# Kernel tuning notes

Hardware: AMD Instinct MI355X
Metric: run time of the kernel (lower is better)

The kernel has to match this reference:

```python
import jax, jax.numpy as jnp
import numpy as np

B, T, IN, OUT = 8, 2048, 1024, 512
DT, TAU = 1.0, 20.0


def setup_inputs() -> dict:
    key = jax.random.key(0)
    k1, k2 = jax.random.split(key)
    x = jax.random.normal(k1, (B, T, IN), jnp.float32)
    lim = 1.0 / np.sqrt(IN)
    weight = jax.random.uniform(k2, (OUT, IN), jnp.float32, -lim, lim)
    bias = jnp.zeros((OUT,), jnp.float32)
    # fixed tau trainer: decay = exp(-dt / tau) per output feature
    decay = jnp.full((OUT,), float(np.exp(-DT / TAU)), jnp.float32)
    return {"input_tensor": x, "weight": weight, "bias": bias, "decay": decay}


def reference(input_tensor, weight, bias, decay):
    # Hoist the time-invariant GEMM out of the recurrence: [B,T,OUT]
    current = jnp.einsum('bti,oi->bto', input_tensor, weight) + bias
    v0 = jnp.zeros((input_tensor.shape[0], weight.shape[0]), input_tensor.dtype)

    def step(v_tm1, c_t):
        v_t = decay * v_tm1 + (1.0 - decay) * c_t
        return v_t, v_t

    # scan over time axis: [T,B,OUT]
    _, outs = jax.lax.scan(step, v0, jnp.swapaxes(current, 0, 1))
    outputs = jnp.swapaxes(outs, 0, 1)  # [B,T,OUT]
    states = jnp.concatenate([v0[:, None, :], outputs], axis=1)[None]  # [1,B,T+1,OUT]
    return outputs, states
```

## Files before the change

kernel.cpp:

```cpp
#include <hip/hip_runtime.h>
#include <hip/hip_bf16.h>
#include <cstddef>
#include <cstdint>

#define BB    8
#define TT    2048
#define KIN   1024
#define NOUT  512
#define CHUNK 32
#define NCHUNK (TT / CHUNK)

#define BM 128
#define BN 64
#define BK 32
#define NKSTEP (KIN / BK)

typedef __attribute__((ext_vector_type(4))) float          f32x4;
typedef __attribute__((ext_vector_type(4))) unsigned int   u32x4;
typedef _Float16 f16x8 __attribute__((ext_vector_type(8)));

__global__ __launch_bounds__(256) void conv_f16_kernel(
    const float* __restrict__ src, _Float16* __restrict__ dst, int n8) {
  int i = blockIdx.x * blockDim.x + threadIdx.x;
  const int stride = gridDim.x * blockDim.x;
  for (; i < n8; i += stride) {
    float4 x0 = reinterpret_cast<const float4*>(src)[2 * i];
    float4 x1 = reinterpret_cast<const float4*>(src)[2 * i + 1];
    f16x8 h;
    h[0] = (_Float16)x0.x; h[1] = (_Float16)x0.y;
    h[2] = (_Float16)x0.z; h[3] = (_Float16)x0.w;
    h[4] = (_Float16)x1.x; h[5] = (_Float16)x1.y;
    h[6] = (_Float16)x1.z; h[7] = (_Float16)x1.w;
    reinterpret_cast<f16x8*>(dst)[i] = h;
  }
}

#define G2L(gp, sp)                                                        \
  __builtin_amdgcn_global_load_lds(                                       \
      (const __attribute__((address_space(1))) void*)(gp),                \
      (__attribute__((address_space(3))) void*)(sp), 16, 0, 0)

__global__ __launch_bounds__(256, 4) void gemm_f16(
    const float* __restrict__ X, const _Float16* __restrict__ Wh,
    const float* __restrict__ bias, const float* __restrict__ decay,
    float* __restrict__ C, float* __restrict__ vend) {
  __shared__ __align__(16) unsigned char smem[8192 + 2 * 4096];

  const int tid  = threadIdx.x;
  const int wave = tid >> 6;
  const int lane = tid & 63;
  const int m0 = blockIdx.x * BM;
  const int n0 = blockIdx.y * BN;
  const int wm = (wave >> 1) * 64;
  const int wn = (wave & 1) * 32;
  const int frow = lane & 15;
  const int g    = lane >> 4;

  const int ar = wave * 8 + (lane >> 3);
  const int as = lane & 7;
  const float* gA = X + (size_t)(m0 + ar) * KIN + as * 4;
  const int awb = ((as >> 1) ^ ((ar >> 1) & 3)) * 16 + (as & 1) * 8;

  const int brow = wave * 16 + (lane >> 2);
  const int sgB  = (lane & 3) ^ ((lane >> 3) & 3);
  const _Float16* gB = Wh + (size_t)(n0 + brow) * KIN + sgB * 8;

  const int swzr = (g ^ ((frow >> 1) & 3)) << 4;

  f32x4 acc[4][2] = {};
  f32x4 ra0, ra1, ra2, ra3;

  ra0 = *reinterpret_cast<const f32x4*>(gA);
  ra1 = *reinterpret_cast<const f32x4*>(gA + (size_t)32 * KIN);
  ra2 = *reinterpret_cast<const f32x4*>(gA + (size_t)64 * KIN);
  ra3 = *reinterpret_cast<const f32x4*>(gA + (size_t)96 * KIN);
  G2L(gB, smem + 8192 + wave * 1024);

  for (int t = 0; t < NKSTEP; ++t) {
    __syncthreads();

    {
      uint2 w;
      w.x = __builtin_bit_cast(unsigned int, __builtin_amdgcn_cvt_pkrtz(ra0[0], ra0[1]));
      w.y = __builtin_bit_cast(unsigned int, __builtin_amdgcn_cvt_pkrtz(ra0[2], ra0[3]));
      *reinterpret_cast<uint2*>(smem + (ar +  0) * 64 + awb) = w;
      w.x = __builtin_bit_cast(unsigned int, __builtin_amdgcn_cvt_pkrtz(ra1[0], ra1[1]));
      w.y = __builtin_bit_cast(unsigned int, __builtin_amdgcn_cvt_pkrtz(ra1[2], ra1[3]));
      *reinterpret_cast<uint2*>(smem + (ar + 32) * 64 + awb) = w;
      w.x = __builtin_bit_cast(unsigned int, __builtin_amdgcn_cvt_pkrtz(ra2[0], ra2[1]));
      w.y = __builtin_bit_cast(unsigned int, __builtin_amdgcn_cvt_pkrtz(ra2[2], ra2[3]));
      *reinterpret_cast<uint2*>(smem + (ar + 64) * 64 + awb) = w;
      w.x = __builtin_bit_cast(unsigned int, __builtin_amdgcn_cvt_pkrtz(ra3[0], ra3[1]));
      w.y = __builtin_bit_cast(unsigned int, __builtin_amdgcn_cvt_pkrtz(ra3[2], ra3[3]));
      *reinterpret_cast<uint2*>(smem + (ar + 96) * 64 + awb) = w;
    }
    __syncthreads();

    if (t + 1 < NKSTEP) {
      const int k0 = (t + 1) * BK;
      ra0 = *reinterpret_cast<const f32x4*>(gA + k0);
      ra1 = *reinterpret_cast<const f32x4*>(gA + (size_t)32 * KIN + k0);
      ra2 = *reinterpret_cast<const f32x4*>(gA + (size_t)64 * KIN + k0);
      ra3 = *reinterpret_cast<const f32x4*>(gA + (size_t)96 * KIN + k0);
      G2L(gB + k0, smem + 8192 + ((t + 1) & 1) * 4096 + wave * 1024);
    }

    const unsigned char* bB = smem + 8192 + (t & 1) * 4096;
    f16x8 af[4];
#pragma unroll
    for (int mi = 0; mi < 4; ++mi)
      af[mi] = *reinterpret_cast<const f16x8*>(smem + (wm + mi * 16 + frow) * 64 + swzr);
#pragma unroll
    for (int ni = 0; ni < 2; ++ni) {
      f16x8 bf = *reinterpret_cast<const f16x8*>(bB + (wn + ni * 16 + frow) * 64 + swzr);
#pragma unroll
      for (int mi = 0; mi < 4; ++mi)
        acc[mi][ni] = __builtin_amdgcn_mfma_f32_16x16x32_f16(af[mi], bf, acc[mi][ni], 0, 0, 0);
    }
  }

  const int colb = n0 + wn + frow;
  const int rowb = m0 + wm + (g << 2);
  const float bv0 = bias[colb];
  const float bv1 = bias[colb + 16];
#pragma unroll
  for (int mi = 0; mi < 4; ++mi) {
#pragma unroll
    for (int r = 0; r < 4; ++r) {
      C[(size_t)(rowb + mi * 16 + r) * NOUT + colb]      = acc[mi][0][r] + bv0;
      C[(size_t)(rowb + mi * 16 + r) * NOUT + colb + 16] = acc[mi][1][r] + bv1;
    }
  }

  {
    const float d0 = decay[colb];
    const float d1 = decay[colb + 16];
    float rr[2][2];
#pragma unroll
    for (int ni = 0; ni < 2; ++ni) {
      const float d = ni ? d1 : d0;
      const float bv = ni ? bv1 : bv0;
      const float omd = 1.0f - d;
      const float dd = d * d, d4 = dd * dd, d8 = d4 * d4;
      const float d16 = d8 * d8, d12 = d8 * d4;
      const float dpg = (g == 0) ? d12 : (g == 1) ? d8 : (g == 2) ? d4 : 1.0f;
      float s[4];
#pragma unroll
      for (int mi = 0; mi < 4; ++mi) {
        float v = acc[mi][ni][0] + bv;
        v = v * d + (acc[mi][ni][1] + bv);
        v = v * d + (acc[mi][ni][2] + bv);
        v = v * d + (acc[mi][ni][3] + bv);
        s[mi] = omd * v;
      }
      float ulo = dpg * (s[0] * d16 + s[1]);
      float uhi = dpg * (s[2] * d16 + s[3]);
      ulo += __shfl_xor(ulo, 16); ulo += __shfl_xor(ulo, 32);
      uhi += __shfl_xor(uhi, 16); uhi += __shfl_xor(uhi, 32);
      rr[0][ni] = ulo; rr[1][ni] = uhi;
    }
    const int b     = m0 >> 11;
    const int clo   = ((m0 & (TT - 1)) >> 5) + (wm >> 5);
    const float val = rr[g >> 1][g & 1];
    const int chunk = clo + (g >> 1);
    const int col   = n0 + wn + frow + (g & 1) * 16;
    vend[((size_t)b * NCHUNK + chunk) * NOUT + col] = val;
  }
}

__global__ __launch_bounds__(256) void gemm_f32_64x64(
    const float* __restrict__ X, const float* __restrict__ W,
    const float* __restrict__ bias, float* __restrict__ C) {
  __shared__ float As[16][65];
  __shared__ float Bs[16][65];
  const int m0  = blockIdx.y * 64;
  const int n0  = blockIdx.x * 64;
  const int tid = threadIdx.x;
  const int tx  = tid & 15;
  const int ty  = tid >> 4;
  const int lr  = tid >> 2;
  const int lk  = (tid & 3) << 2;
  float acc[4][4] = {};
  const float* xa = X + (size_t)(m0 + lr) * KIN + lk;
  const float* wb = W + (size_t)(n0 + lr) * KIN + lk;
  for (int k0 = 0; k0 < KIN; k0 += 16) {
    float4 av = *reinterpret_cast<const float4*>(xa + k0);
    float4 bv = *reinterpret_cast<const float4*>(wb + k0);
    As[lk + 0][lr] = av.x; As[lk + 1][lr] = av.y;
    As[lk + 2][lr] = av.z; As[lk + 3][lr] = av.w;
    Bs[lk + 0][lr] = bv.x; Bs[lk + 1][lr] = bv.y;
    Bs[lk + 2][lr] = bv.z; Bs[lk + 3][lr] = bv.w;
    __syncthreads();
#pragma unroll
    for (int k = 0; k < 16; ++k) {
      float a[4], b[4];
#pragma unroll
      for (int i = 0; i < 4; ++i) a[i] = As[k][ty * 4 + i];
#pragma unroll
      for (int j = 0; j < 4; ++j) b[j] = Bs[k][tx * 4 + j];
#pragma unroll
      for (int i = 0; i < 4; ++i)
#pragma unroll
        for (int j = 0; j < 4; ++j) acc[i][j] += a[i] * b[j];
    }
    __syncthreads();
  }
  const int n = n0 + tx * 4;
  float4 bv = *reinterpret_cast<const float4*>(&bias[n]);
#pragma unroll
  for (int i = 0; i < 4; ++i) {
    const int m = m0 + ty * 4 + i;
    float4 r;
    r.x = acc[i][0] + bv.x; r.y = acc[i][1] + bv.y;
    r.z = acc[i][2] + bv.z; r.w = acc[i][3] + bv.w;
    *reinterpret_cast<float4*>(&C[(size_t)m * NOUT + n]) = r;
  }
}

__global__ __launch_bounds__(512) void scan_chunks(
    const float* __restrict__ vend, const float* __restrict__ decay,
    float* __restrict__ vinit) {
  const int b = blockIdx.x;
  const int o = threadIdx.x;
  const float d = decay[o];
  float d2 = d * d, d4 = d2 * d2, d8 = d4 * d4, d16 = d8 * d8;
  const float dL = d16 * d16;
  float V = 0.0f;
  for (int c = 0; c < NCHUNK; ++c) {
    const size_t idx = ((size_t)b * NCHUNK + c) * NOUT + o;
    vinit[idx] = V;
    V = dL * V + vend[idx];
  }
}

__global__ __launch_bounds__(512) void scan_fixup(
    float* __restrict__ C, float* __restrict__ states,
    const float* __restrict__ decay, const float* __restrict__ vinit) {
  const int b = blockIdx.x / NCHUNK;
  const int c = blockIdx.x % NCHUNK;
  const int o = threadIdx.x;
  const float d   = decay[o];
  const float omd = 1.0f - d;
  float v = vinit[((size_t)b * NCHUNK + c) * NOUT + o];
  size_t obase = ((size_t)b * TT + (size_t)c * CHUNK) * NOUT + o;
  size_t sbase = ((size_t)b * (TT + 1) + (size_t)c * CHUNK + 1) * NOUT + o;
#pragma unroll 4
  for (int k = 0; k < CHUNK; ++k) {
    v = d * v + omd * C[obase + (size_t)k * NOUT];
    C[obase + (size_t)k * NOUT]      = v;
    states[sbase + (size_t)k * NOUT] = v;
  }
  if (c == 0) states[((size_t)b * (TT + 1)) * NOUT + o] = 0.0f;
}

__global__ __launch_bounds__(512) void scan_seq(
    float* __restrict__ C, float* __restrict__ states,
    const float* __restrict__ decay) {
  const int b = blockIdx.x;
  const int o = threadIdx.x;
  const float d   = decay[o];
  const float omd = 1.0f - d;
  float v = 0.0f;
  states[((size_t)b * (TT + 1)) * NOUT + o] = 0.0f;
  for (int t = 0; t < TT; ++t) {
    const size_t oi = ((size_t)b * TT + t) * NOUT + o;
    float x = C[oi];
    v = d * v + omd * x;
    C[oi] = v;
    states[((size_t)b * (TT + 1) + t + 1) * NOUT + o] = v;
  }
}

extern "C" void kernel_launch(void* const* d_in, const int* in_sizes, int n_in,
                              void* d_out, int out_size, void* d_ws, size_t ws_size,
                              hipStream_t stream) {
  const float* x     = (const float*)d_in[0];
  const float* w     = (const float*)d_in[1];
  const float* bias  = (const float*)d_in[2];
  const float* decay = (const float*)d_in[3];

  float* out    = (float*)d_out;
  float* states = out + (size_t)BB * TT * NOUT;

  const size_t szW = (size_t)NOUT * KIN;
  const size_t scan_elems = (size_t)BB * NCHUNK * NOUT;
  const size_t need = szW * sizeof(_Float16)
                    + 2 * scan_elems * sizeof(float);

  if (ws_size >= need) {
    _Float16* Wh = (_Float16*)d_ws;
    float* vend  = (float*)(Wh + szW);
    float* vinit = vend + scan_elems;

    conv_f16_kernel<<<256, 256, 0, stream>>>(w, Wh, (int)(szW / 8));
    gemm_f16<<<dim3((BB * TT) / BM, NOUT / BN), 256, 0, stream>>>(
        x, Wh, bias, decay, out, vend);
    scan_chunks<<<BB, NOUT, 0, stream>>>(vend, decay, vinit);
    scan_fixup <<<BB * NCHUNK, NOUT, 0, stream>>>(out, states, decay, vinit);
  } else {
    gemm_f32_64x64<<<dim3(NOUT / 64, (BB * TT) / 64), 256, 0, stream>>>(x, w, bias, out);
    scan_seq<<<BB, NOUT, 0, stream>>>(out, states, decay);
  }
}
```

Before: 76.68 us.

## Double-buffer A and B tiles in LDS with two-stage register prefetch

```diff
diff --git a/kernel.cpp b/kernel.cpp
--- a/kernel.cpp
+++ b/kernel.cpp
@@ -14,6 +14,9 @@
 #define BN 64
 #define BK 32
 #define NKSTEP (KIN / BK)
+
+#define ABUF 8192
+#define BBUF 4096
 
 typedef __attribute__((ext_vector_type(4))) float          f32x4;
 typedef __attribute__((ext_vector_type(4))) unsigned int   u32x4;
@@ -35,16 +38,11 @@
   }
 }
 
-#define G2L(gp, sp)                                                        \
-  __builtin_amdgcn_global_load_lds(                                       \
-      (const __attribute__((address_space(1))) void*)(gp),                \
-      (__attribute__((address_space(3))) void*)(sp), 16, 0, 0)
-
 __global__ __launch_bounds__(256, 4) void gemm_f16(
     const float* __restrict__ X, const _Float16* __restrict__ Wh,
     const float* __restrict__ bias, const float* __restrict__ decay,
     float* __restrict__ C, float* __restrict__ vend) {
-  __shared__ __align__(16) unsigned char smem[8192 + 2 * 4096];
+  __shared__ __align__(16) unsigned char smem[2 * ABUF + 2 * BBUF];
 
   const int tid  = threadIdx.x;
   const int wave = tid >> 6;
@@ -56,67 +54,92 @@
   const int frow = lane & 15;
   const int g    = lane >> 4;
 
+  unsigned char* bufA0 = smem;
+  unsigned char* bufA1 = smem + ABUF;
+  unsigned char* bufB0 = smem + 2 * ABUF;
+  unsigned char* bufB1 = smem + 2 * ABUF + BBUF;
+
   const int ar = wave * 8 + (lane >> 3);
   const int as = lane & 7;
   const float* gA = X + (size_t)(m0 + ar) * KIN + as * 4;
   const int awb = ((as >> 1) ^ ((ar >> 1) & 3)) * 16 + (as & 1) * 8;
 
-  const int brow = wave * 16 + (lane >> 2);
-  const int sgB  = (lane & 3) ^ ((lane >> 3) & 3);
-  const _Float16* gB = Wh + (size_t)(n0 + brow) * KIN + sgB * 8;
+  const int br = wave * 16 + (lane >> 2);
+  const int sb = lane & 3;
+  const _Float16* gB = Wh + (size_t)(n0 + br) * KIN + (sb ^ ((br >> 1) & 3)) * 8;
+  const int bwb = br * 64 + sb * 16;
 
   const int swzr = (g ^ ((frow >> 1) & 3)) << 4;
 
   f32x4 acc[4][2] = {};
-  f32x4 ra0, ra1, ra2, ra3;
-
-  ra0 = *reinterpret_cast<const f32x4*>(gA);
-  ra1 = *reinterpret_cast<const f32x4*>(gA + (size_t)32 * KIN);
-  ra2 = *reinterpret_cast<const f32x4*>(gA + (size_t)64 * KIN);
-  ra3 = *reinterpret_cast<const f32x4*>(gA + (size_t)96 * KIN);
-  G2L(gB, smem + 8192 + wave * 1024);
-
-  for (int t = 0; t < NKSTEP; ++t) {
-    __syncthreads();
-
-    {
-      uint2 w;
-      w.x = __builtin_bit_cast(unsigned int, __builtin_amdgcn_cvt_pkrtz(ra0[0], ra0[1]));
-      w.y = __builtin_bit_cast(unsigned int, __builtin_amdgcn_cvt_pkrtz(ra0[2], ra0[3]));
-      *reinterpret_cast<uint2*>(smem + (ar +  0) * 64 + awb) = w;
-      w.x = __builtin_bit_cast(unsigned int, __builtin_amdgcn_cvt_pkrtz(ra1[0], ra1[1]));
-      w.y = __builtin_bit_cast(unsigned int, __builtin_amdgcn_cvt_pkrtz(ra1[2], ra1[3]));
-      *reinterpret_cast<uint2*>(smem + (ar + 32) * 64 + awb) = w;
-      w.x = __builtin_bit_cast(unsigned int, __builtin_amdgcn_cvt_pkrtz(ra2[0], ra2[1]));
-      w.y = __builtin_bit_cast(unsigned int, __builtin_amdgcn_cvt_pkrtz(ra2[2], ra2[3]));
-      *reinterpret_cast<uint2*>(smem + (ar + 64) * 64 + awb) = w;
-      w.x = __builtin_bit_cast(unsigned int, __builtin_amdgcn_cvt_pkrtz(ra3[0], ra3[1]));
-      w.y = __builtin_bit_cast(unsigned int, __builtin_amdgcn_cvt_pkrtz(ra3[2], ra3[3]));
-      *reinterpret_cast<uint2*>(smem + (ar + 96) * 64 + awb) = w;
-    }
-    __syncthreads();
-
-    if (t + 1 < NKSTEP) {
-      const int k0 = (t + 1) * BK;
-      ra0 = *reinterpret_cast<const f32x4*>(gA + k0);
-      ra1 = *reinterpret_cast<const f32x4*>(gA + (size_t)32 * KIN + k0);
-      ra2 = *reinterpret_cast<const f32x4*>(gA + (size_t)64 * KIN + k0);
-      ra3 = *reinterpret_cast<const f32x4*>(gA + (size_t)96 * KIN + k0);
-      G2L(gB + k0, smem + 8192 + ((t + 1) & 1) * 4096 + wave * 1024);
-    }
-
-    const unsigned char* bB = smem + 8192 + (t & 1) * 4096;
-    f16x8 af[4];
-#pragma unroll
-    for (int mi = 0; mi < 4; ++mi)
-      af[mi] = *reinterpret_cast<const f16x8*>(smem + (wm + mi * 16 + frow) * 64 + swzr);
-#pragma unroll
-    for (int ni = 0; ni < 2; ++ni) {
-      f16x8 bf = *reinterpret_cast<const f16x8*>(bB + (wn + ni * 16 + frow) * 64 + swzr);
-#pragma unroll
-      for (int mi = 0; mi < 4; ++mi)
-        acc[mi][ni] = __builtin_amdgcn_mfma_f32_16x16x32_f16(af[mi], bf, acc[mi][ni], 0, 0, 0);
-    }
+
+  f32x4 rA0_a, rA1_a, rA2_a, rA3_a;  u32x4 rB_a;
+  f32x4 rA0_b, rA1_b, rA2_b, rA3_b;  u32x4 rB_b;
+
+#define LOADSET(S, k0)                                                        \
+  do {                                                                        \
+    rA0_##S = *reinterpret_cast<const f32x4*>(gA + (k0));                     \
+    rA1_##S = *reinterpret_cast<const f32x4*>(gA + (size_t)32 * KIN + (k0));  \
+    rA2_##S = *reinterpret_cast<const f32x4*>(gA + (size_t)64 * KIN + (k0));  \
+    rA3_##S = *reinterpret_cast<const f32x4*>(gA + (size_t)96 * KIN + (k0));  \
+    rB_##S  = *reinterpret_cast<const u32x4*>(gB + (k0));                     \
+  } while (0)
+
+#define STORESET(S, dA, dB)                                                   \
+  do {                                                                        \
+    uint2 w;                                                                  \
+    w.x = __builtin_bit_cast(unsigned int, __builtin_amdgcn_cvt_pkrtz(rA0_##S[0], rA0_##S[1])); \
+    w.y = __builtin_bit_cast(unsigned int, __builtin_amdgcn_cvt_pkrtz(rA0_##S[2], rA0_##S[3])); \
+    *reinterpret_cast<uint2*>((dA) + (ar +  0) * 64 + awb) = w;               \
+    w.x = __builtin_bit_cast(unsigned int, __builtin_amdgcn_cvt_pkrtz(rA1_##S[0], rA1_##S[1])); \
+    w.y = __builtin_bit_cast(unsigned int, __builtin_amdgcn_cvt_pkrtz(rA1_##S[2], rA1_##S[3])); \
+    *reinterpret_cast<uint2*>((dA) + (ar + 32) * 64 + awb) = w;               \
+    w.x = __builtin_bit_cast(unsigned int, __builtin_amdgcn_cvt_pkrtz(rA2_##S[0], rA2_##S[1])); \
+    w.y = __builtin_bit_cast(unsigned int, __builtin_amdgcn_cvt_pkrtz(rA2_##S[2], rA2_##S[3])); \
+    *reinterpret_cast<uint2*>((dA) + (ar + 64) * 64 + awb) = w;               \
+    w.x = __builtin_bit_cast(unsigned int, __builtin_amdgcn_cvt_pkrtz(rA3_##S[0], rA3_##S[1])); \
+    w.y = __builtin_bit_cast(unsigned int, __builtin_amdgcn_cvt_pkrtz(rA3_##S[2], rA3_##S[3])); \
+    *reinterpret_cast<uint2*>((dA) + (ar + 96) * 64 + awb) = w;               \
+    *reinterpret_cast<u32x4*>((dB) + bwb) = rB_##S;                           \
+  } while (0)
+
+#define COMPUTE(cA, cB)                                                       \
+  do {                                                                        \
+    f16x8 af[4];                                                              \
+    _Pragma("unroll")                                                         \
+    for (int mi = 0; mi < 4; ++mi)                                            \
+      af[mi] = *reinterpret_cast<const f16x8*>((cA) + (wm + mi * 16 + frow) * 64 + swzr); \
+    _Pragma("unroll")                                                         \
+    for (int ni = 0; ni < 2; ++ni) {                                          \
+      f16x8 bf = *reinterpret_cast<const f16x8*>((cB) + (wn + ni * 16 + frow) * 64 + swzr); \
+      _Pragma("unroll")                                                       \
+      for (int mi = 0; mi < 4; ++mi)                                          \
+        acc[mi][ni] = __builtin_amdgcn_mfma_f32_16x16x32_f16(af[mi], bf, acc[mi][ni], 0, 0, 0); \
+    }                                                                         \
+  } while (0)
+
+#define BARRIER()                                                             \
+  do {                                                                        \
+    asm volatile("s_waitcnt lgkmcnt(0)" ::: "memory");                        \
+    __builtin_amdgcn_s_barrier();                                             \
+  } while (0)
+
+  LOADSET(a, 0);
+  LOADSET(b, BK);
+  STORESET(a, bufA0, bufB0);
+  LOADSET(a, 2 * BK);
+  BARRIER();
+
+  for (int tt = 0; tt < NKSTEP; tt += 2) {
+    STORESET(b, bufA1, bufB1);
+    if (tt + 3 < NKSTEP) LOADSET(b, (tt + 3) * BK);
+    COMPUTE(bufA0, bufB0);
+    BARRIER();
+
+    if (tt + 2 < NKSTEP) STORESET(a, bufA0, bufB0);
+    if (tt + 4 < NKSTEP) LOADSET(a, (tt + 4) * BK);
+    COMPUTE(bufA1, bufB1);
+    BARRIER();
   }
 
   const int colb = n0 + wn + frow;
```

After: 73.28 us. 4.4% less time.

## Pre-convert X and W to f16 in pre-swizzled tile layout, widen BN to 128

Applied to the files above, without the earlier changes.

```diff
diff --git a/kernel.cpp b/kernel.cpp
--- a/kernel.cpp
+++ b/kernel.cpp
@@ -11,27 +11,34 @@
 #define NCHUNK (TT / CHUNK)
 
 #define BM 128
-#define BN 64
+#define BN 128
 #define BK 32
 #define NKSTEP (KIN / BK)
+#define TILEB 8192
 
 typedef __attribute__((ext_vector_type(4))) float          f32x4;
 typedef __attribute__((ext_vector_type(4))) unsigned int   u32x4;
 typedef _Float16 f16x8 __attribute__((ext_vector_type(8)));
 
-__global__ __launch_bounds__(256) void conv_f16_kernel(
-    const float* __restrict__ src, _Float16* __restrict__ dst, int n8) {
-  int i = blockIdx.x * blockDim.x + threadIdx.x;
+__global__ __launch_bounds__(256) void conv_tiled_f16(
+    const float* __restrict__ src, unsigned char* __restrict__ dst, int total) {
+  int idx = blockIdx.x * blockDim.x + threadIdx.x;
   const int stride = gridDim.x * blockDim.x;
-  for (; i < n8; i += stride) {
-    float4 x0 = reinterpret_cast<const float4*>(src)[2 * i];
-    float4 x1 = reinterpret_cast<const float4*>(src)[2 * i + 1];
+  for (; idx < total; idx += stride) {
+    const int r  = idx >> 7;
+    const int s8 = idx & 127;
+    const float* p = src + (size_t)r * KIN + s8 * 8;
+    float4 a = *reinterpret_cast<const float4*>(p);
+    float4 b = *reinterpret_cast<const float4*>(p + 4);
     f16x8 h;
-    h[0] = (_Float16)x0.x; h[1] = (_Float16)x0.y;
-    h[2] = (_Float16)x0.z; h[3] = (_Float16)x0.w;
-    h[4] = (_Float16)x1.x; h[5] = (_Float16)x1.y;
-    h[6] = (_Float16)x1.z; h[7] = (_Float16)x1.w;
-    reinterpret_cast<f16x8*>(dst)[i] = h;
+    h[0] = (_Float16)a.x; h[1] = (_Float16)a.y;
+    h[2] = (_Float16)a.z; h[3] = (_Float16)a.w;
+    h[4] = (_Float16)b.x; h[5] = (_Float16)b.y;
+    h[6] = (_Float16)b.z; h[7] = (_Float16)b.w;
+    const int row  = r & 127;
+    const int tile = (r >> 7) * NKSTEP + (s8 >> 2);
+    const int slot = (s8 & 3) ^ ((row >> 1) & 3);
+    *reinterpret_cast<f16x8*>(dst + (size_t)tile * TILEB + row * 64 + slot * 16) = h;
   }
 }
 
@@ -40,11 +47,11 @@
       (const __attribute__((address_space(1))) void*)(gp),                \
       (__attribute__((address_space(3))) void*)(sp), 16, 0, 0)
 
-__global__ __launch_bounds__(256, 4) void gemm_f16(
-    const float* __restrict__ X, const _Float16* __restrict__ Wh,
+__global__ __launch_bounds__(256, 2) void gemm_f16(
+    const unsigned char* __restrict__ Xt, const unsigned char* __restrict__ Wt,
     const float* __restrict__ bias, const float* __restrict__ decay,
     float* __restrict__ C, float* __restrict__ vend) {
-  __shared__ __align__(16) unsigned char smem[8192 + 2 * 4096];
+  __shared__ __align__(16) unsigned char smem[2 * TILEB];
 
   const int tid  = threadIdx.x;
   const int wave = tid >> 6;
@@ -52,67 +59,37 @@
   const int m0 = blockIdx.x * BM;
   const int n0 = blockIdx.y * BN;
   const int wm = (wave >> 1) * 64;
-  const int wn = (wave & 1) * 32;
+  const int wn = (wave & 1) * 64;
   const int frow = lane & 15;
   const int g    = lane >> 4;
 
-  const int ar = wave * 8 + (lane >> 3);
-  const int as = lane & 7;
-  const float* gA = X + (size_t)(m0 + ar) * KIN + as * 4;
-  const int awb = ((as >> 1) ^ ((ar >> 1) & 3)) * 16 + (as & 1) * 8;
-
-  const int brow = wave * 16 + (lane >> 2);
-  const int sgB  = (lane & 3) ^ ((lane >> 3) & 3);
-  const _Float16* gB = Wh + (size_t)(n0 + brow) * KIN + sgB * 8;
+  unsigned char* sA = smem;
+  unsigned char* sB = smem + TILEB;
+
+  const unsigned char* srcA = Xt + (size_t)(m0 >> 7) * NKSTEP * TILEB + tid * 16;
+  const unsigned char* srcB = Wt + (size_t)(n0 >> 7) * NKSTEP * TILEB + tid * 16;
+  const int ldsw = wave * 1024;
 
   const int swzr = (g ^ ((frow >> 1) & 3)) << 4;
 
-  f32x4 acc[4][2] = {};
-  f32x4 ra0, ra1, ra2, ra3;
-
-  ra0 = *reinterpret_cast<const f32x4*>(gA);
-  ra1 = *reinterpret_cast<const f32x4*>(gA + (size_t)32 * KIN);
-  ra2 = *reinterpret_cast<const f32x4*>(gA + (size_t)64 * KIN);
-  ra3 = *reinterpret_cast<const f32x4*>(gA + (size_t)96 * KIN);
-  G2L(gB, smem + 8192 + wave * 1024);
+  f32x4 acc[4][4] = {};
 
   for (int t = 0; t < NKSTEP; ++t) {
     __syncthreads();
-
-    {
-      uint2 w;
-      w.x = __builtin_bit_cast(unsigned int, __builtin_amdgcn_cvt_pkrtz(ra0[0], ra0[1]));
-      w.y = __builtin_bit_cast(unsigned int, __builtin_amdgcn_cvt_pkrtz(ra0[2], ra0[3]));
-      *reinterpret_cast<uint2*>(smem + (ar +  0) * 64 + awb) = w;
-      w.x = __builtin_bit_cast(unsigned int, __builtin_amdgcn_cvt_pkrtz(ra1[0], ra1[1]));
-      w.y = __builtin_bit_cast(unsigned int, __builtin_amdgcn_cvt_pkrtz(ra1[2], ra1[3]));
-      *reinterpret_cast<uint2*>(smem + (ar + 32) * 64 + awb) = w;
-      w.x = __builtin_bit_cast(unsigned int, __builtin_amdgcn_cvt_pkrtz(ra2[0], ra2[1]));
-      w.y = __builtin_bit_cast(unsigned int, __builtin_amdgcn_cvt_pkrtz(ra2[2], ra2[3]));
-      *reinterpret_cast<uint2*>(smem + (ar + 64) * 64 + awb) = w;
-      w.x = __builtin_bit_cast(unsigned int, __builtin_amdgcn_cvt_pkrtz(ra3[0], ra3[1]));
-      w.y = __builtin_bit_cast(unsigned int, __builtin_amdgcn_cvt_pkrtz(ra3[2], ra3[3]));
-      *reinterpret_cast<uint2*>(smem + (ar + 96) * 64 + awb) = w;
-    }
-    __syncthreads();
-
-    if (t + 1 < NKSTEP) {
-      const int k0 = (t + 1) * BK;
-      ra0 = *reinterpret_cast<const f32x4*>(gA + k0);
-      ra1 = *reinterpret_cast<const f32x4*>(gA + (size_t)32 * KIN + k0);
-      ra2 = *reinterpret_cast<const f32x4*>(gA + (size_t)64 * KIN + k0);
-      ra3 = *reinterpret_cast<const f32x4*>(gA + (size_t)96 * KIN + k0);
-      G2L(gB + k0, smem + 8192 + ((t + 1) & 1) * 4096 + wave * 1024);
-    }
-
-    const unsigned char* bB = smem + 8192 + (t & 1) * 4096;
+    const size_t toff = (size_t)t * TILEB;
+    G2L(srcA + toff,        sA + ldsw);
+    G2L(srcA + toff + 4096, sA + 4096 + ldsw);
+    G2L(srcB + toff,        sB + ldsw);
+    G2L(srcB + toff + 4096, sB + 4096 + ldsw);
+    __syncthreads();
+
     f16x8 af[4];
 #pragma unroll
     for (int mi = 0; mi < 4; ++mi)
-      af[mi] = *reinterpret_cast<const f16x8*>(smem + (wm + mi * 16 + frow) * 64 + swzr);
-#pragma unroll
-    for (int ni = 0; ni < 2; ++ni) {
-      f16x8 bf = *reinterpret_cast<const f16x8*>(bB + (wn + ni * 16 + frow) * 64 + swzr);
+      af[mi] = *reinterpret_cast<const f16x8*>(sA + (wm + mi * 16 + frow) * 64 + swzr);
+#pragma unroll
+    for (int ni = 0; ni < 4; ++ni) {
+      f16x8 bf = *reinterpret_cast<const f16x8*>(sB + (wn + ni * 16 + frow) * 64 + swzr);
 #pragma unroll
       for (int mi = 0; mi < 4; ++mi)
         acc[mi][ni] = __builtin_amdgcn_mfma_f32_16x16x32_f16(af[mi], bf, acc[mi][ni], 0, 0, 0);
@@ -121,25 +98,25 @@
 
   const int colb = n0 + wn + frow;
   const int rowb = m0 + wm + (g << 2);
-  const float bv0 = bias[colb];
-  const float bv1 = bias[colb + 16];
+  float bv[4];
+#pragma unroll
+  for (int ni = 0; ni < 4; ++ni) bv[ni] = bias[colb + ni * 16];
 #pragma unroll
   for (int mi = 0; mi < 4; ++mi) {
 #pragma unroll
     for (int r = 0; r < 4; ++r) {
-      C[(size_t)(rowb + mi * 16 + r) * NOUT + colb]      = acc[mi][0][r] + bv0;
-      C[(size_t)(rowb + mi * 16 + r) * NOUT + colb + 16] = acc[mi][1][r] + bv1;
+#pragma unroll
+      for (int ni = 0; ni < 4; ++ni)
+        C[(size_t)(rowb + mi * 16 + r) * NOUT + colb + ni * 16] = acc[mi][ni][r] + bv[ni];
     }
   }
 
   {
-    const float d0 = decay[colb];
-    const float d1 = decay[colb + 16];
-    float rr[2][2];
-#pragma unroll
-    for (int ni = 0; ni < 2; ++ni) {
-      const float d = ni ? d1 : d0;
-      const float bv = ni ? bv1 : bv0;
+    float rlo[4], rhi[4];
+#pragma unroll
+    for (int ni = 0; ni < 4; ++ni) {
+      const float d  = decay[colb + ni * 16];
+      const float bb = bv[ni];
       const float omd = 1.0f - d;
       const float dd = d * d, d4 = dd * dd, d8 = d4 * d4;
       const float d16 = d8 * d8, d12 = d8 * d4;
@@ -147,24 +124,29 @@
       float s[4];
 #pragma unroll
       for (int mi = 0; mi < 4; ++mi) {
-        float v = acc[mi][ni][0] + bv;
-        v = v * d + (acc[mi][ni][1] + bv);
-        v = v * d + (acc[mi][ni][2] + bv);
-        v = v * d + (acc[mi][ni][3] + bv);
+        float v = acc[mi][ni][0] + bb;
+        v = v * d + (acc[mi][ni][1] + bb);
+        v = v * d + (acc[mi][ni][2] + bb);
+        v = v * d + (acc[mi][ni][3] + bb);
         s[mi] = omd * v;
       }
       float ulo = dpg * (s[0] * d16 + s[1]);
       float uhi = dpg * (s[2] * d16 + s[3]);
       ulo += __shfl_xor(ulo, 16); ulo += __shfl_xor(ulo, 32);
       uhi += __shfl_xor(uhi, 16); uhi += __shfl_xor(uhi, 32);
-      rr[0][ni] = ulo; rr[1][ni] = uhi;
-    }
-    const int b     = m0 >> 11;
-    const int clo   = ((m0 & (TT - 1)) >> 5) + (wm >> 5);
-    const float val = rr[g >> 1][g & 1];
+      rlo[ni] = ulo; rhi[ni] = uhi;
+    }
+    const int b   = m0 >> 11;
+    const int clo = ((m0 & (TT - 1)) >> 5) + (wm >> 5);
     const int chunk = clo + (g >> 1);
-    const int col   = n0 + wn + frow + (g & 1) * 16;
-    vend[((size_t)b * NCHUNK + chunk) * NOUT + col] = val;
+    const int half  = g >> 1;
+    const int nia   = g & 1;
+    const float v1 = half ? (nia ? rhi[1] : rhi[0]) : (nia ? rlo[1] : rlo[0]);
+    const float v2 = half ? (nia ? rhi[3] : rhi[2]) : (nia ? rlo[3] : rlo[2]);
+    const int col1 = n0 + wn + frow + nia * 16;
+    float* vp = vend + ((size_t)b * NCHUNK + chunk) * NOUT;
+    vp[col1]      = v1;
+    vp[col1 + 32] = v2;
   }
 }
 
@@ -282,19 +264,21 @@
   float* out    = (float*)d_out;
   float* states = out + (size_t)BB * TT * NOUT;
 
-  const size_t szW = (size_t)NOUT * KIN;
+  const size_t szXb = (size_t)BB * TT * KIN * sizeof(_Float16);
+  const size_t szWb = (size_t)NOUT * KIN * sizeof(_Float16);
   const size_t scan_elems = (size_t)BB * NCHUNK * NOUT;
-  const size_t need = szW * sizeof(_Float16)
-                    + 2 * scan_elems * sizeof(float);
+  const size_t need = szXb + szWb + 2 * scan_elems * sizeof(float);
 
   if (ws_size >= need) {
-    _Float16* Wh = (_Float16*)d_ws;
-    float* vend  = (float*)(Wh + szW);
+    unsigned char* Xt = (unsigned char*)d_ws;
+    unsigned char* Wt = Xt + szXb;
+    float* vend  = (float*)(Wt + szWb);
     float* vinit = vend + scan_elems;
 
-    conv_f16_kernel<<<256, 256, 0, stream>>>(w, Wh, (int)(szW / 8));
+    conv_tiled_f16<<<2048, 256, 0, stream>>>(x, Xt, BB * TT * (KIN / 8));
+    conv_tiled_f16<<<256,  256, 0, stream>>>(w, Wt, NOUT * (KIN / 8));
     gemm_f16<<<dim3((BB * TT) / BM, NOUT / BN), 256, 0, stream>>>(
-        x, Wh, bias, decay, out, vend);
+        Xt, Wt, bias, decay, out, vend);
     scan_chunks<<<BB, NOUT, 0, stream>>>(vend, decay, vinit);
     scan_fixup <<<BB * NCHUNK, NOUT, 0, stream>>>(out, states, decay, vinit);
   } else {
```

After: 71.17 us. 7.2% less time.
